# Performance work log

Hardware: AMD Instinct MI355X
Metric: run time of the kernel (lower is better)

The kernel has to match this reference:

```python
import jax, jax.numpy as jnp
import numpy as np

N_NODES = 100000
N_EDGES = 1600000
D_IN, D_HID, D_LAT = 128, 128, 64


def setup_inputs() -> dict:
    key = jax.random.key(0)
    ks = jax.random.split(key, 8)
    x = jax.random.normal(ks[0], (N_NODES, D_IN), dtype=jnp.float32)
    edge_index = jax.random.randint(ks[1], (2, N_EDGES), 0, N_NODES, dtype=jnp.int64)
    s1 = 1.0 / np.sqrt(D_IN)
    s2 = 1.0 / np.sqrt(D_HID)
    return {
        "x": x,
        "edge_index": edge_index,
        "W1_l": jax.random.normal(ks[2], (D_IN, D_HID), dtype=jnp.float32) * s1,
        "W1_r": jax.random.normal(ks[3], (D_IN, D_HID), dtype=jnp.float32) * s1,
        "b1": jnp.zeros((D_HID,), dtype=jnp.float32),
        "W2_l": jax.random.normal(ks[4], (D_HID, D_LAT), dtype=jnp.float32) * s2,
        "W2_r": jax.random.normal(ks[5], (D_HID, D_LAT), dtype=jnp.float32) * s2,
        "b2": jnp.zeros((D_LAT,), dtype=jnp.float32),
    }


def _sage_conv_mean(x, src, dst, W_l, W_r, b):
    """PyG SAGEConv with mean aggregation: lin_l(mean_j x_j) + lin_r(x_i)."""
    n = x.shape[0]
    # scatter-mean of source features into destination nodes
    agg = jax.ops.segment_sum(x[src], dst, num_segments=n)           # [N, d]
    deg = jax.ops.segment_sum(jnp.ones_like(dst, dtype=x.dtype), dst, num_segments=n)
    mean = agg / jnp.maximum(deg, 1.0)[:, None]
    return mean @ W_l + b + x @ W_r


def reference(x, edge_index, W1_l, W1_r, b1, W2_l, W2_r, b2):
    src, dst = edge_index[0], edge_index[1]
    h = jax.nn.relu(_sage_conv_mean(x, src, dst, W1_l, W1_r, b1))
    # Dropout(p=0.2) is identity in eval mode
    z = jax.nn.relu(_sage_conv_mean(h, src, dst, W2_l, W2_r, b2))
    return z
```

## Files before the change

### kernel.cpp

```cpp
#include <hip/hip_runtime.h>

#define N_NODES 100000
#define N_EDGES 1600000
#define D_IN 128
#define D_HID 128
#define D_LAT 64

#define BSHIFT 8
#define NB 392
#define CAP 4608
#define EPB 4096
#define PART_BLOCKS ((N_EDGES + EPB - 1) / EPB)
#define CVT_BLOCKS (((long)N_NODES * 128 / 16 + 255) / 256)

typedef unsigned short ushort_t;
typedef unsigned int uint_t;
typedef unsigned char uchar_t;
using bf16x8 = __attribute__((ext_vector_type(8))) short;
using f32x4  = __attribute__((ext_vector_type(4))) float;
using f32x2  = __attribute__((ext_vector_type(2))) float;

__device__ inline ushort_t f2bf(float f) {
    uint_t u = __float_as_uint(f);
    return (ushort_t)((u + 0x7fffu + ((u >> 16) & 1u)) >> 16);
}
__device__ inline uint_t pack2bf(float a, float b) {
    return (uint_t)f2bf(a) | ((uint_t)f2bf(b) << 16);
}
__device__ inline float bf2f(ushort_t u) {
    return __uint_as_float(((uint_t)u) << 16);
}

#if __has_builtin(__builtin_amdgcn_cvt_pk_f32_fp8) && __has_builtin(__builtin_amdgcn_cvt_pk_fp8_f32)
#define HW_FP8 1
template<bool HI>
__device__ inline f32x2 fp8pk2f(uint_t v) {
    return __builtin_amdgcn_cvt_pk_f32_fp8(v, HI);
}
__device__ inline uint_t f2fp8pk4(float a, float b, float c, float d) {
    uint_t w = __builtin_amdgcn_cvt_pk_fp8_f32(a, b, 0, false);
    w = __builtin_amdgcn_cvt_pk_fp8_f32(c, d, w, true);
    return w;
}
__device__ inline uchar_t f2fp8_byte(float f) {
    return (uchar_t)(__builtin_amdgcn_cvt_pk_fp8_f32(f, f, 0, false) & 0xff);
}
#else
__device__ inline float fp8b2f(uint_t b) {
    uint_t em = b & 0x7f;
    if (em == 0) return 0.f;
    uint_t bits = ((em << 20) + (120u << 23)) | ((b & 0x80u) << 24);
    return __uint_as_float(bits);
}
template<bool HI>
__device__ inline f32x2 fp8pk2f(uint_t v) {
    uint_t w = HI ? (v >> 16) : v;
    f32x2 r; r.x = fp8b2f(w & 0xff); r.y = fp8b2f((w >> 8) & 0xff);
    return r;
}
__device__ inline uint_t f2fp8_1(float f) {
    uint_t u = __float_as_uint(f);
    uint_t s = (u >> 31) << 7;
    uint_t au = u & 0x7fffffff;
    if (au >= 0x43e00000u) return s | 0x7e;
    if (au < 0x3c000000u) return s;
    uint_t r = au + 0x0007ffffu + ((au >> 20) & 1u);
    return s | (((r >> 20) - (120u << 3)) & 0x7f);
}
__device__ inline uint_t f2fp8pk4(float a, float b, float c, float d) {
    return f2fp8_1(a) | (f2fp8_1(b) << 8) | (f2fp8_1(c) << 16) | (f2fp8_1(d) << 24);
}
__device__ inline uchar_t f2fp8_byte(float f) { return (uchar_t)f2fp8_1(f); }
#endif

__device__ inline void accf8x4p(f32x2* a, uint_t w, int b2) {
    a[b2]     += fp8pk2f<false>(w);
    a[b2 + 1] += fp8pk2f<true>(w);
}
__device__ inline void accf8x16p(f32x2* a, uint4 u) {
    accf8x4p(a, u.x, 0); accf8x4p(a, u.y, 2); accf8x4p(a, u.z, 4); accf8x4p(a, u.w, 6);
}

template<int RSHIFT, int NV, int STRIDE, int D>
__device__ inline void gather_tail_step(const uchar_t* __restrict__ base,
                                        const int* __restrict__ idxp,
                                        int n, int& k, f32x2* acc) {
    if (k + D <= n) {
        int idt[D];
        #pragma unroll
        for (int j = 0; j < D; ++j) idt[j] = idxp[(k + j) * STRIDE];
        uint4 u[D][NV];
        #pragma unroll
        for (int j = 0; j < D; ++j) {
            #pragma unroll
            for (int v = 0; v < NV; ++v)
                u[j][v] = *(const uint4*)(base + ((long)idt[j] << RSHIFT) + v * 16);
        }
        #pragma unroll
        for (int j = 0; j < D; ++j) {
            #pragma unroll
            for (int v = 0; v < NV; ++v)
                accf8x16p(acc + v * 8, u[j][v]);
        }
        k += D;
    }
}

template<int RSHIFT, int NV, int DEPTH, int STRIDE = 1>
__device__ inline void gather_acc_fp8n(const uchar_t* __restrict__ base,
                                       const int* __restrict__ idxp,
                                       int n, f32x2* acc) {
    int k = 0;
    int idx[DEPTH];
    if (n >= DEPTH) {
        #pragma unroll
        for (int j = 0; j < DEPTH; ++j) idx[j] = idxp[j * STRIDE];
    }
    while (k + DEPTH <= n) {
        uint4 u[DEPTH][NV];
        #pragma unroll
        for (int j = 0; j < DEPTH; ++j) {
            #pragma unroll
            for (int v = 0; v < NV; ++v)
                u[j][v] = *(const uint4*)(base + ((long)idx[j] << RSHIFT) + v * 16);
        }
        int kn = k + DEPTH;
        if (kn + DEPTH <= n) {
            #pragma unroll
            for (int j = 0; j < DEPTH; ++j) idx[j] = idxp[(kn + j) * STRIDE];
        }
        #pragma unroll
        for (int j = 0; j < DEPTH; ++j) {
            #pragma unroll
            for (int v = 0; v < NV; ++v)
                accf8x16p(acc + v * 8, u[j][v]);
        }
        k = kn;
    }
    gather_tail_step<RSHIFT, NV, STRIDE, 4>(base, idxp, n, k, acc);
    gather_tail_step<RSHIFT, NV, STRIDE, 2>(base, idxp, n, k, acc);
    gather_tail_step<RSHIFT, NV, STRIDE, 1>(base, idxp, n, k, acc);
}

__device__ inline void pack_w256(const float* Wl, const float* Wr, ushort_t* pack,
                                 int N, int tid) {
    int lane = tid & 63;
    int t = tid >> 6;
    int kt = t & 7;
    int nt = t >> 3;
    int n = nt * 16 + (lane & 15);
    int kbase = kt * 32 + (lane >> 4) * 8;
    ushort_t v[8];
    #pragma unroll
    for (int j = 0; j < 8; ++j) {
        int k = kbase + j;
        float w = (k < 128) ? Wl[k * N + n] : Wr[(k - 128) * N + n];
        v[j] = f2bf(w);
    }
    *(uint4*)(pack + (long)tid * 8) = *(uint4*)v;
}
__device__ inline void pack_w128(const float* W, ushort_t* pack, int N, int tid) {
    int lane = tid & 63;
    int t = tid >> 6;
    int kt = t & 3;
    int nt = t >> 2;
    int n = nt * 16 + (lane & 15);
    int kbase = kt * 32 + (lane >> 4) * 8;
    ushort_t v[8];
    #pragma unroll
    for (int j = 0; j < 8; ++j) v[j] = f2bf(W[(kbase + j) * N + n]);
    *(uint4*)(pack + (long)tid * 8) = *(uint4*)v;
}

__global__ __launch_bounds__(256) void prep_kernel(
        const float* __restrict__ W1_l, const float* __restrict__ W1_r,
        ushort_t* __restrict__ pack1,
        const float* __restrict__ W2_l, ushort_t* __restrict__ pack2l,
        const float* __restrict__ W2_r, ushort_t* __restrict__ pack2r,
        int* __restrict__ gCur,
        const float* __restrict__ x, ushort_t* __restrict__ xb,
        uchar_t* __restrict__ x8) {
    int b = blockIdx.x;
    if (b < 16) {
        pack_w256(W1_l, W1_r, pack1, 128, b * 256 + threadIdx.x);
    } else if (b < 20) {
        pack_w128(W2_l, pack2l, 64, (b - 16) * 256 + threadIdx.x);
    } else if (b < 24) {
        pack_w128(W2_r, pack2r, 64, (b - 20) * 256 + threadIdx.x);
    } else if (b < 26) {
        int t = (b - 24) * 256 + threadIdx.x;
        if (t < NB) gCur[t] = t * CAP;
    } else {
        long i = ((long)(b - 26) * 256 + threadIdx.x) * 16;
        if (i >= (long)N_NODES * 128) return;
        float4 a = *(const float4*)(x + i);
        float4 bb = *(const float4*)(x + i + 4);
        float4 c = *(const float4*)(x + i + 8);
        float4 d = *(const float4*)(x + i + 12);
        uint4 ob0, ob1;
        ob0.x = pack2bf(a.x, a.y);  ob0.y = pack2bf(a.z, a.w);
        ob0.z = pack2bf(bb.x, bb.y); ob0.w = pack2bf(bb.z, bb.w);
        ob1.x = pack2bf(c.x, c.y);  ob1.y = pack2bf(c.z, c.w);
        ob1.z = pack2bf(d.x, d.y);  ob1.w = pack2bf(d.z, d.w);
        *(uint4*)(xb + i) = ob0;
        *(uint4*)(xb + i + 8) = ob1;
        uint4 o8;
        o8.x = f2fp8pk4(a.x, a.y, a.z, a.w);
        o8.y = f2fp8pk4(bb.x, bb.y, bb.z, bb.w);
        o8.z = f2fp8pk4(c.x, c.y, c.z, c.w);
        o8.w = f2fp8pk4(d.x, d.y, d.z, d.w);
        *(uint4*)(x8 + i) = o8;
    }
}

__global__ __launch_bounds__(256) void bucket_scatter_kernel(const int* __restrict__ src,
                                                             const int* __restrict__ dst,
                                                             int* __restrict__ gCur,
                                                             int* __restrict__ bedges) {
    __shared__ int h[NB];
    __shared__ int start[NB];
    for (int j = threadIdx.x; j < NB; j += 256) h[j] = 0;
    __syncthreads();
    long base = (long)blockIdx.x * EPB + threadIdx.x * 16;
    int dc[16], sc[16];
    int cnt = 0;
    if (base + 16 <= N_EDGES) {
        #pragma unroll
        for (int j = 0; j < 4; ++j) {
            int4 d4 = *(const int4*)(dst + base + j * 4);
            int4 s4 = *(const int4*)(src + base + j * 4);
            dc[j * 4 + 0] = d4.x; dc[j * 4 + 1] = d4.y; dc[j * 4 + 2] = d4.z; dc[j * 4 + 3] = d4.w;
            sc[j * 4 + 0] = s4.x; sc[j * 4 + 1] = s4.y; sc[j * 4 + 2] = s4.z; sc[j * 4 + 3] = s4.w;
        }
        cnt = 16;
    } else if (base < N_EDGES) {
        cnt = (int)(N_EDGES - base);
        for (int j = 0; j < cnt; ++j) { dc[j] = dst[base + j]; sc[j] = src[base + j]; }
    }
    for (int j = 0; j < cnt; ++j) atomicAdd(&h[dc[j] >> BSHIFT], 1);
    __syncthreads();
    for (int j = threadIdx.x; j < NB; j += 256)
        start[j] = h[j] ? atomicAdd(&gCur[j], h[j]) : 0;
    __syncthreads();
    for (int j = 0; j < cnt; ++j) {
        int b = dc[j] >> BSHIFT;
        int p = atomicAdd(&start[b], 1);
        if (p < (b + 1) * CAP)
            bedges[p] = ((dc[j] & 255) << 24) | sc[j];
    }
}

__global__ __launch_bounds__(256) void bucket_sort_kernel(const int* __restrict__ gCur,
                                                          const int* __restrict__ bedges,
                                                          int* __restrict__ csr,
                                                          int2* __restrict__ off2) {
    __shared__ int sdata[256];
    __shared__ int cur[256];
    int b = blockIdx.x, t = threadIdx.x;
    int r0 = b * CAP;
    int n = gCur[b] - r0;
    if (n > CAP) n = CAP;
    cur[t] = 0;
    __syncthreads();
    for (int k = t * 4; k < n; k += 1024) {
        int4 v4 = *(const int4*)(bedges + r0 + k);
        int m = n - k;
        atomicAdd(&cur[(unsigned)v4.x >> 24], 1);
        if (m > 1) atomicAdd(&cur[(unsigned)v4.y >> 24], 1);
        if (m > 2) atomicAdd(&cur[(unsigned)v4.z >> 24], 1);
        if (m > 3) atomicAdd(&cur[(unsigned)v4.w >> 24], 1);
    }
    __syncthreads();
    int c = cur[t];
    sdata[t] = c;
    __syncthreads();
    for (int d = 1; d < 256; d <<= 1) {
        int u = (t >= d) ? sdata[t - d] : 0;
        __syncthreads();
        sdata[t] += u;
        __syncthreads();
    }
    int ex = (t == 0) ? 0 : sdata[t - 1];
    off2[(b << BSHIFT) + t] = make_int2(r0 + ex, c);
    cur[t] = ex;
    __syncthreads();
    for (int k = t * 4; k < n; k += 1024) {
        int4 v4 = *(const int4*)(bedges + r0 + k);
        int m = n - k;
        {
            int p = atomicAdd(&cur[(unsigned)v4.x >> 24], 1);
            csr[r0 + p] = v4.x & 0xFFFFFF;
        }
        if (m > 1) {
            int p = atomicAdd(&cur[(unsigned)v4.y >> 24], 1);
            csr[r0 + p] = v4.y & 0xFFFFFF;
        }
        if (m > 2) {
            int p = atomicAdd(&cur[(unsigned)v4.z >> 24], 1);
            csr[r0 + p] = v4.z & 0xFFFFFF;
        }
        if (m > 3) {
            int p = atomicAdd(&cur[(unsigned)v4.w >> 24], 1);
            csr[r0 + p] = v4.w & 0xFFFFFF;
        }
    }
}

#define HSTRIDE 132
__global__ __launch_bounds__(256) void mfma_mlp_fused_kernel(
        const int2* __restrict__ off2, const int* __restrict__ csr_src,
        const uchar_t* __restrict__ x8,
        const ushort_t* __restrict__ Ax,
        const ushort_t* __restrict__ pack1, const float* __restrict__ bias,
        const ushort_t* __restrict__ pack2l, const ushort_t* __restrict__ pack2r,
        ushort_t* __restrict__ f2, uchar_t* __restrict__ g8) {
    __shared__ ushort_t mtile[32 * HSTRIDE];
    __shared__ ushort_t htile[32 * HSTRIDE];
    long m0b = (long)blockIdx.x * 32;
    {
        int lane8 = threadIdx.x & 7;
        int local = threadIdx.x >> 3;
        long i = m0b + local;
        int2 bd = off2[i];
        const uchar_t* gbase = x8 + lane8 * 16;
        f32x2 acc2[8];
        #pragma unroll
        for (int j = 0; j < 8; ++j) acc2[j] = (f32x2){0.f, 0.f};
        gather_acc_fp8n<7, 1, 8, 1>(gbase, csr_src + bd.x, bd.y, acc2);
        float* pa = (float*)acc2;
        float inv = (bd.y > 0) ? 1.f / (float)bd.y : 0.f;
        uint4 o0, o1;
        o0.x = pack2bf(pa[0] * inv,  pa[1] * inv);
        o0.y = pack2bf(pa[2] * inv,  pa[3] * inv);
        o0.z = pack2bf(pa[4] * inv,  pa[5] * inv);
        o0.w = pack2bf(pa[6] * inv,  pa[7] * inv);
        o1.x = pack2bf(pa[8] * inv,  pa[9] * inv);
        o1.y = pack2bf(pa[10] * inv, pa[11] * inv);
        o1.z = pack2bf(pa[12] * inv, pa[13] * inv);
        o1.w = pack2bf(pa[14] * inv, pa[15] * inv);
        ushort_t* mp = mtile + local * HSTRIDE + lane8 * 16;
        *(uint4*)mp = o0;
        *(uint4*)(mp + 8) = o1;
    }
    __syncthreads();
    int lane = threadIdx.x & 63;
    int wave = threadIdx.x >> 6;
    int wr = wave & 1;
    int wc = wave >> 1;
    int r = lane & 15;
    int quad = lane >> 4;
    int rowl = wr * 16 + r;
    long arow = m0b + rowl;

    bf16x8 areg[8];
    #pragma unroll
    for (int kt = 0; kt < 8; ++kt) {
        int k = (kt & 3) * 32 + quad * 8;
        areg[kt] = (kt < 4)
            ? *(const bf16x8*)(&mtile[rowl * HSTRIDE + k])
            : *(const bf16x8*)(Ax + arow * 128 + k);
    }

    f32x4 acc[4];
    #pragma unroll
    for (int nt = 0; nt < 4; ++nt) acc[nt] = (f32x4){0.f, 0.f, 0.f, 0.f};
    #pragma unroll
    for (int nt = 0; nt < 4; ++nt) {
        int gnt = wc * 4 + nt;
        #pragma unroll
        for (int kt = 0; kt < 8; ++kt) {
            bf16x8 bfrag = *(const bf16x8*)(pack1 + ((long)(gnt * 8 + kt) * 64 + lane) * 8);
            acc[nt] = __builtin_amdgcn_mfma_f32_16x16x32_bf16(areg[kt], bfrag, acc[nt], 0, 0, 0);
        }
    }

    #pragma unroll
    for (int nt = 0; nt < 4; ++nt) {
        int col = wc * 64 + nt * 16 + r;
        float bj = bias[col];
        #pragma unroll
        for (int q = 0; q < 4; ++q) {
            float v = fmaxf(acc[nt][q] + bj, 0.f);
            htile[(wr * 16 + quad * 4 + q) * HSTRIDE + col] = f2bf(v);
        }
    }
    __syncthreads();
    bf16x8 areg2[4];
    #pragma unroll
    for (int kt = 0; kt < 4; ++kt)
        areg2[kt] = *(const bf16x8*)(&htile[rowl * HSTRIDE + kt * 32 + quad * 8]);
    f32x4 gacc[2];
    #pragma unroll
    for (int nt = 0; nt < 2; ++nt) gacc[nt] = (f32x4){0.f, 0.f, 0.f, 0.f};
    #pragma unroll
    for (int nt = 0; nt < 2; ++nt) {
        int gnt = wc * 2 + nt;
        #pragma unroll
        for (int kt = 0; kt < 4; ++kt) {
            bf16x8 bfrag = *(const bf16x8*)(pack2l + ((long)(gnt * 4 + kt) * 64 + lane) * 8);
            gacc[nt] = __builtin_amdgcn_mfma_f32_16x16x32_bf16(areg2[kt], bfrag, gacc[nt], 0, 0, 0);
        }
    }
    #pragma unroll
    for (int nt = 0; nt < 2; ++nt) {
        int col = wc * 32 + nt * 16 + r;
        #pragma unroll
        for (int q = 0; q < 4; ++q) {
            long orow = m0b + wr * 16 + quad * 4 + q;
            g8[orow * 64 + col] = f2fp8_byte(gacc[nt][q]);
        }
    }
    f32x4 facc[2];
    #pragma unroll
    for (int nt = 0; nt < 2; ++nt) facc[nt] = (f32x4){0.f, 0.f, 0.f, 0.f};
    #pragma unroll
    for (int nt = 0; nt < 2; ++nt) {
        int gnt = wc * 2 + nt;
        #pragma unroll
        for (int kt = 0; kt < 4; ++kt) {
            bf16x8 bfrag = *(const bf16x8*)(pack2r + ((long)(gnt * 4 + kt) * 64 + lane) * 8);
            facc[nt] = __builtin_amdgcn_mfma_f32_16x16x32_bf16(areg2[kt], bfrag, facc[nt], 0, 0, 0);
        }
    }
    #pragma unroll
    for (int nt = 0; nt < 2; ++nt) {
        int col = wc * 32 + nt * 16 + r;
        #pragma unroll
        for (int q = 0; q < 4; ++q) {
            long orow = m0b + wr * 16 + quad * 4 + q;
            f2[orow * 64 + col] = f2bf(facc[nt][q]);
        }
    }
}

__global__ __launch_bounds__(256) void final_gather_kernel(
        const int2* __restrict__ off2, const int* __restrict__ csr_src,
        const uchar_t* __restrict__ g8,
        const ushort_t* __restrict__ f2, const float* __restrict__ b2,
        float* __restrict__ out) {
    int lane8 = threadIdx.x & 7;
    int d = lane8 & 3;
    int p = lane8 >> 2;
    int local = threadIdx.x >> 3;
    long i = (long)blockIdx.x * 32 + local;
    int2 bd = off2[i];
    int n = bd.y;
    const uchar_t* base = g8 + d * 16;
    f32x2 acc2[8];
    #pragma unroll
    for (int j = 0; j < 8; ++j) acc2[j] = (f32x2){0.f, 0.f};
    int np = (n + 1 - p) >> 1;
    gather_acc_fp8n<6, 1, 8, 2>(base, csr_src + bd.x + p, np, acc2);
    float* pa = (float*)acc2;
    #pragma unroll
    for (int j = 0; j < 16; ++j) pa[j] += __shfl_xor(pa[j], 4);
    float inv = (n > 0) ? 1.f / (float)n : 0.f;
    int dim0 = d * 16 + p * 8;
    ushort_t fu[8];
    *(uint4*)fu = *(const uint4*)(f2 + i * 64 + dim0);
    float o[8];
    #pragma unroll
    for (int j = 0; j < 8; ++j) {
        float m = bf2f(f2bf(pa[p * 8 + j] * inv));
        o[j] = fmaxf(m + bf2f(fu[j]) + b2[dim0 + j], 0.f);
    }
    *(float4*)(out + i * 64 + dim0)     = make_float4(o[0], o[1], o[2], o[3]);
    *(float4*)(out + i * 64 + dim0 + 4) = make_float4(o[4], o[5], o[6], o[7]);
}

extern "C" void kernel_launch(void* const* d_in, const int* in_sizes, int n_in,
                              void* d_out, int out_size, void* d_ws, size_t ws_size,
                              hipStream_t stream) {
    const float* x    = (const float*)d_in[0];
    const int*   ei   = (const int*)d_in[1];
    const float* W1_l = (const float*)d_in[2];
    const float* W1_r = (const float*)d_in[3];
    const float* b1   = (const float*)d_in[4];
    const float* W2_l = (const float*)d_in[5];
    const float* W2_r = (const float*)d_in[6];
    const float* b2   = (const float*)d_in[7];
    float* out = (float*)d_out;

    const int* src = ei;
    const int* dst = ei + N_EDGES;

    int*  gCur   = (int*)d_ws;
    int2* off2   = (int2*)(gCur + 512);
    int*  bedges = (int*)(off2 + 100608);
    int*  csr    = bedges + NB * CAP;
    ushort_t* xb = (ushort_t*)(csr + NB * CAP);
    uchar_t*  x8 = (uchar_t*)(xb + (long)N_NODES * 128);
    ushort_t* f2 = (ushort_t*)(x8 + (long)N_NODES * 128);
    ushort_t* pack1  = f2 + (long)N_NODES * 64;
    ushort_t* pack2l = pack1 + 256 * 128;
    ushort_t* pack2r = pack2l + 128 * 64;
    uchar_t*  g8     = (uchar_t*)(pack2r + 128 * 64);

    prep_kernel<<<26 + CVT_BLOCKS, 256, 0, stream>>>(
        W1_l, W1_r, pack1, W2_l, pack2l, W2_r, pack2r, gCur, x, xb, x8);

    bucket_scatter_kernel<<<PART_BLOCKS, 256, 0, stream>>>(src, dst, gCur, bedges);
    bucket_sort_kernel<<<NB, 256, 0, stream>>>(gCur, bedges, csr, off2);

    mfma_mlp_fused_kernel<<<N_NODES / 32, 256, 0, stream>>>(
        off2, csr, x8, xb, pack1, b1, pack2l, pack2r, f2, g8);

    final_gather_kernel<<<N_NODES / 32, 256, 0, stream>>>(
        off2, csr, g8, f2, b2, out);
}
```

Measured before the change: 224.5 us.

## Merge bucket scatter into prep kernel using relative bucket counters

Folds the edge bucket-scatter pass into the prep kernel as extra blocks, so the scatter runs concurrently with the weight packing and x conversion instead of as a separate launch. The global bucket cursors become relative counts zeroed by a memset, which removes the dependency on prep initializing them. The final gather also hoists the f2 and bias loads ahead of the gather loop so their latency overlaps. The cost is an added memset launch and larger LDS and register use in the merged prep kernel.

```diff
diff --git a/kernel.cpp b/kernel.cpp
--- a/kernel.cpp
+++ b/kernel.cpp
@@ -12,6 +12,10 @@
 #define EPB 4096
 #define PART_BLOCKS ((N_EDGES + EPB - 1) / EPB)
 #define CVT_BLOCKS (((long)N_NODES * 128 / 16 + 255) / 256)
+#define PK1_BASE PART_BLOCKS
+#define PK2L_BASE (PK1_BASE + 16)
+#define PK2R_BASE (PK2L_BASE + 4)
+#define CVT_BASE (PK2R_BASE + 4)
 
 typedef unsigned short ushort_t;
 typedef unsigned int uint_t;
@@ -173,25 +177,55 @@
 }
 
 __global__ __launch_bounds__(256) void prep_kernel(
+        const int* __restrict__ src, const int* __restrict__ dst,
+        int* __restrict__ gCurRel, int* __restrict__ bedges,
         const float* __restrict__ W1_l, const float* __restrict__ W1_r,
         ushort_t* __restrict__ pack1,
         const float* __restrict__ W2_l, ushort_t* __restrict__ pack2l,
         const float* __restrict__ W2_r, ushort_t* __restrict__ pack2r,
-        int* __restrict__ gCur,
         const float* __restrict__ x, ushort_t* __restrict__ xb,
         uchar_t* __restrict__ x8) {
     int b = blockIdx.x;
-    if (b < 16) {
-        pack_w256(W1_l, W1_r, pack1, 128, b * 256 + threadIdx.x);
-    } else if (b < 20) {
-        pack_w128(W2_l, pack2l, 64, (b - 16) * 256 + threadIdx.x);
-    } else if (b < 24) {
-        pack_w128(W2_r, pack2r, 64, (b - 20) * 256 + threadIdx.x);
-    } else if (b < 26) {
-        int t = (b - 24) * 256 + threadIdx.x;
-        if (t < NB) gCur[t] = t * CAP;
+    if (b < PART_BLOCKS) {
+        __shared__ int h[NB];
+        __shared__ int start[NB];
+        for (int j = threadIdx.x; j < NB; j += 256) h[j] = 0;
+        __syncthreads();
+        long base = (long)b * EPB + threadIdx.x * 16;
+        int dc[16], sc[16];
+        int cnt = 0;
+        if (base + 16 <= N_EDGES) {
+            #pragma unroll
+            for (int j = 0; j < 4; ++j) {
+                int4 d4 = *(const int4*)(dst + base + j * 4);
+                int4 s4 = *(const int4*)(src + base + j * 4);
+                dc[j * 4 + 0] = d4.x; dc[j * 4 + 1] = d4.y; dc[j * 4 + 2] = d4.z; dc[j * 4 + 3] = d4.w;
+                sc[j * 4 + 0] = s4.x; sc[j * 4 + 1] = s4.y; sc[j * 4 + 2] = s4.z; sc[j * 4 + 3] = s4.w;
+            }
+            cnt = 16;
+        } else if (base < N_EDGES) {
+            cnt = (int)(N_EDGES - base);
+            for (int j = 0; j < cnt; ++j) { dc[j] = dst[base + j]; sc[j] = src[base + j]; }
+        }
+        for (int j = 0; j < cnt; ++j) atomicAdd(&h[dc[j] >> BSHIFT], 1);
+        __syncthreads();
+        for (int j = threadIdx.x; j < NB; j += 256)
+            start[j] = h[j] ? (j * CAP + atomicAdd(&gCurRel[j], h[j])) : 0;
+        __syncthreads();
+        for (int j = 0; j < cnt; ++j) {
+            int bk = dc[j] >> BSHIFT;
+            int p = atomicAdd(&start[bk], 1);
+            if (p < (bk + 1) * CAP)
+                bedges[p] = ((dc[j] & 255) << 24) | sc[j];
+        }
+    } else if (b < PK2L_BASE) {
+        pack_w256(W1_l, W1_r, pack1, 128, (b - PK1_BASE) * 256 + threadIdx.x);
+    } else if (b < PK2R_BASE) {
+        pack_w128(W2_l, pack2l, 64, (b - PK2L_BASE) * 256 + threadIdx.x);
+    } else if (b < CVT_BASE) {
+        pack_w128(W2_r, pack2r, 64, (b - PK2R_BASE) * 256 + threadIdx.x);
     } else {
-        long i = ((long)(b - 26) * 256 + threadIdx.x) * 16;
+        long i = ((long)(b - CVT_BASE) * 256 + threadIdx.x) * 16;
         if (i >= (long)N_NODES * 128) return;
         float4 a = *(const float4*)(x + i);
         float4 bb = *(const float4*)(x + i + 4);
@@ -213,44 +247,7 @@
     }
 }
 
-__global__ __launch_bounds__(256) void bucket_scatter_kernel(const int* __restrict__ src,
-                                                             const int* __restrict__ dst,
-                                                             int* __restrict__ gCur,
-                                                             int* __restrict__ bedges) {
-    __shared__ int h[NB];
-    __shared__ int start[NB];
-    for (int j = threadIdx.x; j < NB; j += 256) h[j] = 0;
-    __syncthreads();
-    long base = (long)blockIdx.x * EPB + threadIdx.x * 16;
-    int dc[16], sc[16];
-    int cnt = 0;
-    if (base + 16 <= N_EDGES) {
-        #pragma unroll
-        for (int j = 0; j < 4; ++j) {
-            int4 d4 = *(const int4*)(dst + base + j * 4);
-            int4 s4 = *(const int4*)(src + base + j * 4);
-            dc[j * 4 + 0] = d4.x; dc[j * 4 + 1] = d4.y; dc[j * 4 + 2] = d4.z; dc[j * 4 + 3] = d4.w;
-            sc[j * 4 + 0] = s4.x; sc[j * 4 + 1] = s4.y; sc[j * 4 + 2] = s4.z; sc[j * 4 + 3] = s4.w;
-        }
-        cnt = 16;
-    } else if (base < N_EDGES) {
-        cnt = (int)(N_EDGES - base);
-        for (int j = 0; j < cnt; ++j) { dc[j] = dst[base + j]; sc[j] = src[base + j]; }
-    }
-    for (int j = 0; j < cnt; ++j) atomicAdd(&h[dc[j] >> BSHIFT], 1);
-    __syncthreads();
-    for (int j = threadIdx.x; j < NB; j += 256)
-        start[j] = h[j] ? atomicAdd(&gCur[j], h[j]) : 0;
-    __syncthreads();
-    for (int j = 0; j < cnt; ++j) {
-        int b = dc[j] >> BSHIFT;
-        int p = atomicAdd(&start[b], 1);
-        if (p < (b + 1) * CAP)
-            bedges[p] = ((dc[j] & 255) << 24) | sc[j];
-    }
-}
-
-__global__ __launch_bounds__(256) void bucket_sort_kernel(const int* __restrict__ gCur,
+__global__ __launch_bounds__(256) void bucket_sort_kernel(const int* __restrict__ gCurRel,
                                                           const int* __restrict__ bedges,
                                                           int* __restrict__ csr,
                                                           int2* __restrict__ off2) {
@@ -258,7 +255,7 @@
     __shared__ int cur[256];
     int b = blockIdx.x, t = threadIdx.x;
     int r0 = b * CAP;
-    int n = gCur[b] - r0;
+    int n = gCurRel[b];
     if (n > CAP) n = CAP;
     cur[t] = 0;
     __syncthreads();
@@ -445,6 +442,11 @@
     long i = (long)blockIdx.x * 32 + local;
     int2 bd = off2[i];
     int n = bd.y;
+    int dim0 = d * 16 + p * 8;
+    ushort_t fu[8];
+    *(uint4*)fu = *(const uint4*)(f2 + i * 64 + dim0);
+    float4 bj0 = *(const float4*)(b2 + dim0);
+    float4 bj1 = *(const float4*)(b2 + dim0 + 4);
     const uchar_t* base = g8 + d * 16;
     f32x2 acc2[8];
     #pragma unroll
@@ -455,14 +457,12 @@
     #pragma unroll
     for (int j = 0; j < 16; ++j) pa[j] += __shfl_xor(pa[j], 4);
     float inv = (n > 0) ? 1.f / (float)n : 0.f;
-    int dim0 = d * 16 + p * 8;
-    ushort_t fu[8];
-    *(uint4*)fu = *(const uint4*)(f2 + i * 64 + dim0);
+    float bja[8] = {bj0.x, bj0.y, bj0.z, bj0.w, bj1.x, bj1.y, bj1.z, bj1.w};
     float o[8];
     #pragma unroll
     for (int j = 0; j < 8; ++j) {
         float m = bf2f(f2bf(pa[p * 8 + j] * inv));
-        o[j] = fmaxf(m + bf2f(fu[j]) + b2[dim0 + j], 0.f);
+        o[j] = fmaxf(m + bf2f(fu[j]) + bja[j], 0.f);
     }
     *(float4*)(out + i * 64 + dim0)     = make_float4(o[0], o[1], o[2], o[3]);
     *(float4*)(out + i * 64 + dim0 + 4) = make_float4(o[4], o[5], o[6], o[7]);
@@ -496,10 +496,11 @@
     ushort_t* pack2r = pack2l + 128 * 64;
     uchar_t*  g8     = (uchar_t*)(pack2r + 128 * 64);
 
-    prep_kernel<<<26 + CVT_BLOCKS, 256, 0, stream>>>(
-        W1_l, W1_r, pack1, W2_l, pack2l, W2_r, pack2r, gCur, x, xb, x8);
-
-    bucket_scatter_kernel<<<PART_BLOCKS, 256, 0, stream>>>(src, dst, gCur, bedges);
+    hipMemsetAsync(gCur, 0, NB * sizeof(int), stream);
+    prep_kernel<<<CVT_BASE + CVT_BLOCKS, 256, 0, stream>>>(
+        src, dst, gCur, bedges,
+        W1_l, W1_r, pack1, W2_l, pack2l, W2_r, pack2r, x, xb, x8);
+
     bucket_sort_kernel<<<NB, 256, 0, stream>>>(gCur, bedges, csr, off2);
 
     mfma_mlp_fused_kernel<<<N_NODES / 32, 256, 0, stream>>>(
```

Measured after the change: 224.1 us, median of 2. Within noise of the previous version (-0.2%).
